# Kernel optimization log

Hardware: AMD Instinct MI355X
Metric: run time of the kernel (lower is better)

Reference implementation:

```python
import jax, jax.numpy as jnp
import numpy as np

B, T = 4, 2048
N_EMBD = 1024
TIME_EMBD = 128
N_HEAD = 16
C_IN = N_EMBD + TIME_EMBD  # 1152


def setup_inputs() -> dict:
    key = jax.random.key(0)
    ks = jax.random.split(key, 7)
    s_in = 1.0 / np.sqrt(C_IN)
    s_e = 1.0 / np.sqrt(N_EMBD)
    return {
        "x": jax.random.normal(ks[0], (B, T, C_IN), jnp.float32),
        "ln_w": jnp.ones((C_IN,), jnp.float32),
        "ln_b": jnp.zeros((C_IN,), jnp.float32),
        "W_attn": jax.random.normal(ks[1], (C_IN, 3 * N_EMBD), jnp.float32) * s_in,
        "b_attn": jax.random.normal(ks[2], (3 * N_EMBD,), jnp.float32) * 0.01,
        "W_proj": jax.random.normal(ks[3], (N_EMBD, N_EMBD), jnp.float32) * s_e,
        "b_proj": jax.random.normal(ks[4], (N_EMBD,), jnp.float32) * 0.01,
    }


def _layernorm(x, w, b, eps=1e-5):
    mu = jnp.mean(x, axis=-1, keepdims=True)
    var = jnp.var(x, axis=-1, keepdims=True)
    return (x - mu) * jax.lax.rsqrt(var + eps) * w + b


def reference(x, ln_w, ln_b, W_attn, b_attn, W_proj, b_proj):
    h = _layernorm(x, ln_w, ln_b)                      # [B,T,C_IN]
    qkv = h @ W_attn + b_attn                          # [B,T,3*N_EMBD]
    q, k, v = jnp.split(qkv, 3, axis=-1)
    hd = N_EMBD // N_HEAD
    q = q.reshape(B, T, N_HEAD, hd).transpose(0, 2, 1, 3)  # [B,H,T,hd]
    k = k.reshape(B, T, N_HEAD, hd).transpose(0, 2, 1, 3)
    v = v.reshape(B, T, N_HEAD, hd).transpose(0, 2, 1, 3)
    att = jnp.einsum("bhqd,bhkd->bhqk", q, k) * (1.0 / np.sqrt(hd))
    mask = jnp.tril(jnp.ones((T, T), bool))
    att = jnp.where(mask, att, -jnp.inf)
    att = jax.nn.softmax(att, axis=-1)                 # dropout p=0 -> identity
    y = jnp.einsum("bhqk,bhkd->bhqd", att, v)          # [B,H,T,hd]
    y = y.transpose(0, 2, 1, 3).reshape(B, T, N_EMBD)
    return y @ W_proj + b_proj
```

## Files before the change

### kernel.cpp

```cpp
#include <hip/hip_runtime.h>
#include <hip/hip_bf16.h>

#define BB 4
#define TT 2048
#define C_IN 1152
#define NE 1024
#define NH 16
#define HD 64
#define MM (BB*TT)
#define N_QKV (3*NE)

typedef __attribute__((ext_vector_type(8))) short s16x8;
typedef __attribute__((ext_vector_type(4))) short s16x4;
typedef __attribute__((ext_vector_type(4))) float f32x4;

static __device__ __forceinline__ unsigned short f2bf(float x) {
    unsigned int u = __float_as_uint(x);
    unsigned int r = (u + 0x7fffu + ((u >> 16) & 1u)) >> 16;
    return (unsigned short)r;
}

static __device__ __forceinline__ void async16(const void* g, void* l) {
    __builtin_amdgcn_global_load_lds((const __attribute__((address_space(1))) void*)g,
                                     (__attribute__((address_space(3))) void*)l, 16, 0, 0);
}

__global__ __launch_bounds__(256) void ln_kernel(const float* __restrict__ x,
                                                 const float* __restrict__ w,
                                                 const float* __restrict__ b,
                                                 unsigned short* __restrict__ h) {
    const int row = blockIdx.x;
    const int tid = threadIdx.x;
    const float4* xr = (const float4*)(x + (size_t)row * C_IN);
    const float4 a0 = xr[tid];
    float4 a1 = make_float4(0.f, 0.f, 0.f, 0.f);
    if (tid < 32) a1 = xr[256 + tid];
    float s  = a0.x + a0.y + a0.z + a0.w + a1.x + a1.y + a1.z + a1.w;
    float sq = a0.x*a0.x + a0.y*a0.y + a0.z*a0.z + a0.w*a0.w
             + a1.x*a1.x + a1.y*a1.y + a1.z*a1.z + a1.w*a1.w;
    for (int off = 1; off < 64; off <<= 1) {
        s  += __shfl_xor(s, off, 64);
        sq += __shfl_xor(sq, off, 64);
    }
    __shared__ float red[2][4];
    const int wid = tid >> 6, lane = tid & 63;
    if (lane == 0) { red[0][wid] = s; red[1][wid] = sq; }
    __syncthreads();
    s  = red[0][0] + red[0][1] + red[0][2] + red[0][3];
    sq = red[1][0] + red[1][1] + red[1][2] + red[1][3];
    const float mu  = s * (1.f / C_IN);
    const float var = sq * (1.f / C_IN) - mu * mu;
    const float rs  = rsqrtf(var + 1e-5f);
    const float4* w4 = (const float4*)w;
    const float4* b4 = (const float4*)b;
    unsigned short* hr = h + (size_t)row * C_IN;
    {
        const float4 wv = w4[tid], bv = b4[tid];
        s16x4 o;
        o[0] = (short)f2bf((a0.x - mu) * rs * wv.x + bv.x);
        o[1] = (short)f2bf((a0.y - mu) * rs * wv.y + bv.y);
        o[2] = (short)f2bf((a0.z - mu) * rs * wv.z + bv.z);
        o[3] = (short)f2bf((a0.w - mu) * rs * wv.w + bv.w);
        *(s16x4*)(hr + tid * 4) = o;
    }
    if (tid < 32) {
        const float4 wv = w4[256 + tid], bv = b4[256 + tid];
        s16x4 o;
        o[0] = (short)f2bf((a1.x - mu) * rs * wv.x + bv.x);
        o[1] = (short)f2bf((a1.y - mu) * rs * wv.y + bv.y);
        o[2] = (short)f2bf((a1.z - mu) * rs * wv.z + bv.z);
        o[3] = (short)f2bf((a1.w - mu) * rs * wv.w + bv.w);
        *(s16x4*)(hr + (256 + tid) * 4) = o;
    }
}

__global__ __launch_bounds__(256) void transpose_cast(const float* __restrict__ in,
                                                      unsigned short* __restrict__ out,
                                                      int K, int N) {
    __shared__ float tile[32][33];
    const int n0 = blockIdx.x * 32, k0 = blockIdx.y * 32;
    const int tx = threadIdx.x & 31, ty = threadIdx.x >> 5;
    for (int i = ty; i < 32; i += 8)
        tile[i][tx] = in[(size_t)(k0 + i) * N + n0 + tx];
    __syncthreads();
    for (int i = ty; i < 32; i += 8)
        out[(size_t)(n0 + i) * K + k0 + tx] = f2bf(tile[tx][i]);
}

#define ATT_SC 0.18033688011112042f

#define EP_STRIDE 136
template <int MODE>
__global__ __launch_bounds__(256) void gemm_bt(const unsigned short* __restrict__ A,
                                               const unsigned short* __restrict__ Bt,
                                               const float* __restrict__ bias,
                                               void* __restrict__ outp,
                                               unsigned short* __restrict__ kb,
                                               unsigned short* __restrict__ vt,
                                               int M, int N, int K) {
    __shared__ unsigned short smem[32768];
    const int tid = threadIdx.x;
    const int wid = tid >> 6, lane = tid & 63;
    const int wm = wid >> 1, wn = wid & 1;
    const int quad = lane >> 4, l16 = lane & 15;

    int m0, n0;
    if (MODE == 0) {
        const int bid = blockIdx.y * gridDim.x + blockIdx.x;
        const int xcd = bid & 7;
        const int k   = bid >> 3;
        const int mg  = k / 96;
        const int r1  = k % 96;
        const int ng  = r1 / 32;
        const int rr  = r1 % 32;
        m0 = (xcd * 8 + mg * 4 + (rr & 3)) * 128;
        n0 = (ng * 8 + (rr >> 2)) * 128;
    } else {
        const int gx  = gridDim.x;
        const int nwg = gx * gridDim.y;
        const int bid = blockIdx.y * gx + blockIdx.x;
        const int wg  = (bid & 7) * (nwg >> 3) + (bid >> 3);
        m0 = (wg / gx) * 128; n0 = (wg % gx) * 128;
    }

    const int rl = lane >> 3;
    const int sc = (lane & 7) ^ rl;
    const unsigned short* gA = A  + (size_t)(m0 + wid * 32 + rl) * K + sc * 8;
    const unsigned short* gB = Bt + (size_t)(n0 + wid * 32 + rl) * K + sc * 8;

    f32x4 acc[4][4] = {};
    const int nk = K >> 6;

    const int sc0 = (quad ^ (l16 & 7)) * 8;
    const int sc1 = ((4 + quad) ^ (l16 & 7)) * 8;

#define STAGE(KT, BUF)                                                          \
    {                                                                           \
        const unsigned short* a_ = gA + (KT) * 64;                              \
        const unsigned short* b_ = gB + (KT) * 64;                              \
        unsigned short* sa_ = &smem[(BUF) * 16384 + wid * 2048];                \
        unsigned short* sb_ = &smem[(BUF) * 16384 + 8192 + wid * 2048];         \
        _Pragma("unroll")                                                       \
        for (int j = 0; j < 4; j++) {                                           \
            async16(a_ + (size_t)(j * 8) * K, sa_ + j * 512);                   \
            async16(b_ + (size_t)(j * 8) * K, sb_ + j * 512);                   \
        }                                                                       \
    }

    STAGE(0, 0);

    for (int kt = 0; kt < nk; kt++) {
        __syncthreads();
        const int cur = kt & 1;
        if (kt + 1 < nk) STAGE(kt + 1, cur ^ 1);

        const unsigned short* As_ = &smem[cur * 16384];
        const unsigned short* Bs_ = &smem[cur * 16384 + 8192];
        #pragma unroll
        for (int h = 0; h < 2; h++) {
            const int sch = h ? sc1 : sc0;
            s16x8 af[4], bfb[4];
            #pragma unroll
            for (int mi = 0; mi < 4; mi++)
                af[mi] = *(const s16x8*)&As_[(wm * 64 + mi * 16 + l16) * 64 + sch];
            #pragma unroll
            for (int ni = 0; ni < 4; ni++)
                bfb[ni] = *(const s16x8*)&Bs_[(wn * 64 + ni * 16 + l16) * 64 + sch];
            #pragma unroll
            for (int mi = 0; mi < 4; mi++)
                #pragma unroll
                for (int ni = 0; ni < 4; ni++)
                    acc[mi][ni] = __builtin_amdgcn_mfma_f32_16x16x32_bf16(af[mi], bfb[ni], acc[mi][ni], 0, 0, 0);
        }
    }
#undef STAGE

    const int which0 = n0 >> 10;
    const float sc_ = (MODE == 0 && which0 == 0) ? ATT_SC : 1.0f;
    for (int ni = 0; ni < 4; ni++) {
        const float bv = bias[n0 + wn * 64 + ni * 16 + l16];
        for (int mi = 0; mi < 4; mi++)
            for (int r = 0; r < 4; r++)
                acc[mi][ni][r] = (acc[mi][ni][r] + bv) * sc_;
    }

    if (MODE == 1) {
        float* Tf = (float*)smem;
        float* out = (float*)outp;
        for (int p = 0; p < 2; p++) {
            __syncthreads();
            if (wm == p) {
                for (int mi = 0; mi < 4; mi++)
                    for (int ni = 0; ni < 4; ni++) {
                        const int col = wn * 64 + ni * 16 + l16;
                        for (int r = 0; r < 4; r++)
                            Tf[(mi * 16 + quad * 4 + r) * 128 + col] = acc[mi][ni][r];
                    }
            }
            __syncthreads();
            const int rlo = tid >> 5;
            const int c4 = (tid & 31) * 4;
            for (int rr2 = rlo; rr2 < 64; rr2 += 8) {
                *(float4*)&out[(size_t)(m0 + p * 64 + rr2) * N + n0 + c4] =
                    *(const float4*)&Tf[rr2 * 128 + c4];
            }
        }
        return;
    }

    const int which = n0 >> 10;
    const int bb = m0 >> 11;
    const int mloc = m0 & 2047;
    unsigned short* T = smem;

    __syncthreads();
    if (which < 2) {
        for (int mi = 0; mi < 4; mi++)
            for (int ni = 0; ni < 4; ni++) {
                const int nl = wn * 64 + ni * 16 + l16;
                for (int r = 0; r < 4; r++)
                    T[(wm * 64 + mi * 16 + quad * 4 + r) * EP_STRIDE + nl] = f2bf(acc[mi][ni][r]);
            }
    } else {
        for (int mi = 0; mi < 4; mi++)
            for (int ni = 0; ni < 4; ni++) {
                const int nlh = wn * 64 + ni * 16 + l16;
                const int mlb = wm * 64 + mi * 16 + quad * 4;
                for (int r = 0; r < 4; r += 2) {
                    const unsigned int pk = (unsigned int)f2bf(acc[mi][ni][r]) |
                                            ((unsigned int)f2bf(acc[mi][ni][r + 1]) << 16);
                    *(unsigned int*)&T[nlh * EP_STRIDE + mlb + r] = pk;
                }
            }
    }
    __syncthreads();

    if (which < 2) {
        unsigned short* qk = (which == 0) ? (unsigned short*)outp : kb;
        const int ml = tid >> 2, c = tid & 3;
        const int nl0 = c * 32;
        const int hh = ((n0 & 1023) >> 6) + (nl0 >> 6);
        const int d0 = nl0 & 63;
        for (int half = 0; half < 2; half++) {
            const int row = half * 64 + ml;
            const int t = mloc + row;
            unsigned short* dst = qk + ((size_t)(bb * 16 + hh) * TT + t) * HD + d0;
            const unsigned short* src = &T[row * EP_STRIDE + nl0];
            for (int u = 0; u < 4; u++)
                *(s16x8*)(dst + u * 8) = *(const s16x8*)(src + u * 8);
        }
    } else {
        const int nlh = tid >> 2, c = tid & 3;
        const int hb = (n0 - 2048) >> 6;
        for (int half = 0; half < 2; half++) {
            const int row = half * 64 + nlh;
            unsigned short* dst = vt + ((size_t)(bb * 16 + hb + half) * HD + nlh) * TT + mloc + c * 32;
            const unsigned short* src = &T[row * EP_STRIDE + c * 32];
            for (int u = 0; u < 4; u++)
                *(s16x8*)(dst + u * 8) = *(const s16x8*)(src + u * 8);
        }
    }
}

#define PST 72

__global__ __launch_bounds__(256) void attn_kernel(const unsigned short* __restrict__ qb,
                                                   const unsigned short* __restrict__ kb,
                                                   const unsigned short* __restrict__ vt,
                                                   unsigned short* __restrict__ yb) {
    __shared__ unsigned short Ks[2][64 * 64];
    __shared__ unsigned short Vs[2][64 * 64];
    __shared__ unsigned short Ps[4][2 * 16 * PST];
    const int tid = threadIdx.x, wid = tid >> 6, lane = tid & 63;
    const int quad = lane >> 4, l16 = lane & 15;
    const int bh = blockIdx.x & 63;
    const int qblk = 15 - (blockIdx.x >> 6);

    const unsigned short* qh = qb + (size_t)bh * TT * HD;
    const unsigned short* kh = kb + (size_t)bh * TT * HD;
    const unsigned short* vh = vt + (size_t)bh * HD * TT;
    unsigned short* ps = Ps[wid];

    const int q0w = qblk * 128 + wid * 32;
    s16x8 aq[2][2];
    #pragma unroll
    for (int mf = 0; mf < 2; mf++) {
        aq[mf][0] = *(const s16x8*)&qh[(size_t)(q0w + mf * 16 + l16) * HD + quad * 8];
        aq[mf][1] = *(const s16x8*)&qh[(size_t)(q0w + mf * 16 + l16) * HD + 32 + quad * 8];
    }
    s16x8 onesf;
    #pragma unroll
    for (int i = 0; i < 8; i++) onesf[i] = (short)0x3F80;

    f32x4 yacc[2][4] = {};
    f32x4 lacc[2] = {};
    const int ntiles = 2 * qblk + 2;

    const int rl = lane >> 3;
    const int cc = (lane & 7) ^ (rl & 7);
    const unsigned short* kp0 = kh + (size_t)(wid * 16 + rl) * HD + cc * 8;
    const unsigned short* kp1 = kh + (size_t)(wid * 16 + 8 + rl) * HD + cc * 8;
    const unsigned short* vp0 = vh + (size_t)(wid * 16 + rl) * TT + cc * 8;
    const unsigned short* vp1 = vh + (size_t)(wid * 16 + 8 + rl) * TT + cc * 8;
    const int ldsK0 = wid * 16 * 64, ldsK1 = (wid * 16 + 8) * 64;

    async16(kp0, &Ks[0][ldsK0]);  async16(kp1, &Ks[0][ldsK1]);
    async16(vp0, &Vs[0][ldsK0]);  async16(vp1, &Vs[0][ldsK1]);
    kp0 += 64 * HD; kp1 += 64 * HD; vp0 += 64; vp1 += 64;

    const int p0s = quad ^ (l16 & 7);
    const int p1s = (4 + quad) ^ (l16 & 7);

#define ATT_STEP(CUR, TT_)                                                              \
    {                                                                                   \
        __syncthreads();                                                                \
        if ((TT_) + 1 < ntiles) {                                                       \
            async16(kp0, &Ks[(CUR) ^ 1][ldsK0]);  async16(kp1, &Ks[(CUR) ^ 1][ldsK1]);  \
            async16(vp0, &Vs[(CUR) ^ 1][ldsK0]);  async16(vp1, &Vs[(CUR) ^ 1][ldsK1]);  \
            kp0 += 64 * HD; kp1 += 64 * HD; vp0 += 64; vp1 += 64;                       \
        }                                                                               \
        const int tk0 = (TT_) * 64;                                                     \
        if (tk0 <= q0w + 31) {                                                          \
            const unsigned short* Kc = Ks[CUR];                                         \
            const unsigned short* Vc = Vs[CUR];                                         \
            s16x8 kf[4][2], vf[4][2];                                                   \
            _Pragma("unroll")                                                           \
            for (int nj = 0; nj < 4; nj++) {                                            \
                kf[nj][0] = *(const s16x8*)&Kc[(nj * 16 + l16) * 64 + p0s * 8];         \
                kf[nj][1] = *(const s16x8*)&Kc[(nj * 16 + l16) * 64 + p1s * 8];         \
            }                                                                           \
            _Pragma("unroll")                                                           \
            for (int ni = 0; ni < 4; ni++) {                                            \
                vf[ni][0] = *(const s16x8*)&Vc[(ni * 16 + l16) * 64 + p0s * 8];         \
                vf[ni][1] = *(const s16x8*)&Vc[(ni * 16 + l16) * 64 + p1s * 8];         \
            }                                                                           \
            _Pragma("unroll")                                                           \
            for (int mf = 0; mf < 2; mf++) {                                            \
                const int f0 = q0w + mf * 16;                                           \
                if (tk0 > f0 + 15) continue;                                            \
                unsigned short* pm = ps + mf * (16 * PST);                              \
                const int qg = f0 + l16;                                                \
                f32x4 st[4];                                                            \
                _Pragma("unroll")                                                       \
                for (int nj = 0; nj < 4; nj++) {                                        \
                    f32x4 z = {};                                                       \
                    z = __builtin_amdgcn_mfma_f32_16x16x32_bf16(kf[nj][0], aq[mf][0], z, 0, 0, 0); \
                    z = __builtin_amdgcn_mfma_f32_16x16x32_bf16(kf[nj][1], aq[mf][1], z, 0, 0, 0); \
                    st[nj] = z;                                                         \
                }                                                                       \
                const bool diag = (tk0 + 64 > f0);                                      \
                float pv[4][4];                                                         \
                _Pragma("unroll")                                                       \
                for (int nj = 0; nj < 4; nj++)                                          \
                    _Pragma("unroll")                                                   \
                    for (int r = 0; r < 4; r++)                                         \
                        pv[nj][r] = exp2f(st[nj][r]);                                   \
                if (diag) {                                                             \
                    _Pragma("unroll")                                                   \
                    for (int nj = 0; nj < 4; nj++) {                                    \
                        const int keyb = tk0 + nj * 16 + quad * 4;                      \
                        _Pragma("unroll")                                               \
                        for (int r = 0; r < 4; r++)                                     \
                            if (keyb + r > qg) pv[nj][r] = 0.f;                         \
                    }                                                                   \
                }                                                                       \
                _Pragma("unroll")                                                       \
                for (int nj = 0; nj < 4; nj++) {                                        \
                    const unsigned int pk0 = __builtin_amdgcn_perm(                     \
                        __float_as_uint(pv[nj][1]), __float_as_uint(pv[nj][0]), 0x07060302u); \
                    const unsigned int pk1 = __builtin_amdgcn_perm(                     \
                        __float_as_uint(pv[nj][3]), __float_as_uint(pv[nj][2]), 0x07060302u); \
                    *(uint2*)&pm[l16 * PST + nj * 16 + quad * 4] = make_uint2(pk0, pk1);\
                }                                                                       \
                __asm volatile("s_waitcnt lgkmcnt(0)" ::: "memory");                    \
                __builtin_amdgcn_s_setprio(1);                                          \
                const s16x8 ap0 = *(const s16x8*)&pm[l16 * PST + quad * 8];             \
                const s16x8 ap1 = *(const s16x8*)&pm[l16 * PST + 32 + quad * 8];        \
                lacc[mf] = __builtin_amdgcn_mfma_f32_16x16x32_bf16(ap0, onesf, lacc[mf], 0, 0, 0); \
                lacc[mf] = __builtin_amdgcn_mfma_f32_16x16x32_bf16(ap1, onesf, lacc[mf], 0, 0, 0); \
                _Pragma("unroll")                                                       \
                for (int ni = 0; ni < 4; ni++) {                                        \
                    yacc[mf][ni] = __builtin_amdgcn_mfma_f32_16x16x32_bf16(ap0, vf[ni][0], yacc[mf][ni], 0, 0, 0); \
                    yacc[mf][ni] = __builtin_amdgcn_mfma_f32_16x16x32_bf16(ap1, vf[ni][1], yacc[mf][ni], 0, 0, 0); \
                }                                                                       \
                __builtin_amdgcn_s_setprio(0);                                          \
            }                                                                           \
        }                                                                               \
    }

    for (int t = 0; t < ntiles; t += 2) {
        ATT_STEP(0, t);
        ATT_STEP(1, t + 1);
    }
#undef ATT_STEP

    const int bbi = bh >> 4, hh = bh & 15;
    #pragma unroll
    for (int mf = 0; mf < 2; mf++) {
        float linv[4];
        #pragma unroll
        for (int r = 0; r < 4; r++)
            linv[r] = 1.0f / lacc[mf][r];
        #pragma unroll
        for (int ni = 0; ni < 4; ni++)
            #pragma unroll
            for (int r = 0; r < 4; r++) {
                const int trow = q0w + mf * 16 + quad * 4 + r;
                yb[((size_t)bbi * TT + trow) * NE + hh * HD + ni * 16 + l16] =
                    f2bf(yacc[mf][ni][r] * linv[r]);
            }
    }
}

extern "C" void kernel_launch(void* const* d_in, const int* in_sizes, int n_in,
                              void* d_out, int out_size, void* d_ws, size_t ws_size,
                              hipStream_t stream) {
    const float* x      = (const float*)d_in[0];
    const float* ln_w   = (const float*)d_in[1];
    const float* ln_b   = (const float*)d_in[2];
    const float* W_attn = (const float*)d_in[3];
    const float* b_attn = (const float*)d_in[4];
    const float* W_proj = (const float*)d_in[5];
    const float* b_proj = (const float*)d_in[6];
    float* out = (float*)d_out;

    char* ws = (char*)d_ws;
    unsigned short* h    = (unsigned short*)ws;  ws += (size_t)MM * C_IN * 2;
    unsigned short* Wat  = (unsigned short*)ws;  ws += (size_t)N_QKV * C_IN * 2;
    unsigned short* Wpt  = (unsigned short*)ws;  ws += (size_t)NE * NE * 2;
    unsigned short* qbuf = (unsigned short*)ws;  ws += (size_t)MM * NE * 2;
    unsigned short* kbuf = (unsigned short*)ws;  ws += (size_t)MM * NE * 2;
    unsigned short* vtbf = (unsigned short*)ws;  ws += (size_t)MM * NE * 2;
    unsigned short* ybuf = (unsigned short*)ws;  ws += (size_t)MM * NE * 2;

    ln_kernel<<<MM, 256, 0, stream>>>(x, ln_w, ln_b, h);
    transpose_cast<<<dim3(N_QKV / 32, C_IN / 32), 256, 0, stream>>>(W_attn, Wat, C_IN, N_QKV);
    transpose_cast<<<dim3(NE / 32, NE / 32), 256, 0, stream>>>(W_proj, Wpt, NE, NE);
    gemm_bt<0><<<dim3(N_QKV / 128, MM / 128), 256, 0, stream>>>(h, Wat, b_attn, qbuf, kbuf, vtbf,
                                                                MM, N_QKV, C_IN);
    attn_kernel<<<64 * 16, 256, 0, stream>>>(qbuf, kbuf, vtbf, ybuf);
    gemm_bt<1><<<dim3(NE / 128, MM / 128), 256, 0, stream>>>(ybuf, Wpt, b_proj, out, nullptr, nullptr,
                                                             MM, NE, NE);
}
```

Before: 288.6 us.

## Merge prep kernels and enlarge attention blocks to 256 queries with 8 waves

LayerNorm and both weight transpose-casts now run in a single launch that dispatches on block index. The attention kernel moves from 256 to 512 threads (8 waves), so each block covers 256 query rows and shares each K/V tile across twice as many waves. The grid shrinks to 512 blocks with a reordered q-block schedule, and each thread issues one async K and one async V load per tile. This halves K/V global traffic per query and removes two launches, at the cost of coarser load balancing across the causal triangle and fewer resident blocks.

```diff
diff --git a/kernel.cpp b/kernel.cpp
--- a/kernel.cpp
+++ b/kernel.cpp
@@ -25,61 +25,76 @@
                                      (__attribute__((address_space(3))) void*)l, 16, 0, 0);
 }
 
-__global__ __launch_bounds__(256) void ln_kernel(const float* __restrict__ x,
-                                                 const float* __restrict__ w,
-                                                 const float* __restrict__ b,
-                                                 unsigned short* __restrict__ h) {
-    const int row = blockIdx.x;
+#define TCA_BLOCKS ((N_QKV / 32) * (C_IN / 32))
+#define TCP_BLOCKS ((NE / 32) * (NE / 32))
+__global__ __launch_bounds__(256) void prep_kernel(const float* __restrict__ x,
+                                                   const float* __restrict__ lw,
+                                                   const float* __restrict__ lb,
+                                                   unsigned short* __restrict__ h,
+                                                   const float* __restrict__ Wa,
+                                                   unsigned short* __restrict__ Wat,
+                                                   const float* __restrict__ Wp,
+                                                   unsigned short* __restrict__ Wpt) {
+    __shared__ float tile[32][33];
+    __shared__ float red[2][4];
+    const int bid = blockIdx.x;
     const int tid = threadIdx.x;
-    const float4* xr = (const float4*)(x + (size_t)row * C_IN);
-    const float4 a0 = xr[tid];
-    float4 a1 = make_float4(0.f, 0.f, 0.f, 0.f);
-    if (tid < 32) a1 = xr[256 + tid];
-    float s  = a0.x + a0.y + a0.z + a0.w + a1.x + a1.y + a1.z + a1.w;
-    float sq = a0.x*a0.x + a0.y*a0.y + a0.z*a0.z + a0.w*a0.w
-             + a1.x*a1.x + a1.y*a1.y + a1.z*a1.z + a1.w*a1.w;
-    for (int off = 1; off < 64; off <<= 1) {
-        s  += __shfl_xor(s, off, 64);
-        sq += __shfl_xor(sq, off, 64);
-    }
-    __shared__ float red[2][4];
-    const int wid = tid >> 6, lane = tid & 63;
-    if (lane == 0) { red[0][wid] = s; red[1][wid] = sq; }
-    __syncthreads();
-    s  = red[0][0] + red[0][1] + red[0][2] + red[0][3];
-    sq = red[1][0] + red[1][1] + red[1][2] + red[1][3];
-    const float mu  = s * (1.f / C_IN);
-    const float var = sq * (1.f / C_IN) - mu * mu;
-    const float rs  = rsqrtf(var + 1e-5f);
-    const float4* w4 = (const float4*)w;
-    const float4* b4 = (const float4*)b;
-    unsigned short* hr = h + (size_t)row * C_IN;
-    {
-        const float4 wv = w4[tid], bv = b4[tid];
-        s16x4 o;
-        o[0] = (short)f2bf((a0.x - mu) * rs * wv.x + bv.x);
-        o[1] = (short)f2bf((a0.y - mu) * rs * wv.y + bv.y);
-        o[2] = (short)f2bf((a0.z - mu) * rs * wv.z + bv.z);
-        o[3] = (short)f2bf((a0.w - mu) * rs * wv.w + bv.w);
-        *(s16x4*)(hr + tid * 4) = o;
-    }
-    if (tid < 32) {
-        const float4 wv = w4[256 + tid], bv = b4[256 + tid];
-        s16x4 o;
-        o[0] = (short)f2bf((a1.x - mu) * rs * wv.x + bv.x);
-        o[1] = (short)f2bf((a1.y - mu) * rs * wv.y + bv.y);
-        o[2] = (short)f2bf((a1.z - mu) * rs * wv.z + bv.z);
-        o[3] = (short)f2bf((a1.w - mu) * rs * wv.w + bv.w);
-        *(s16x4*)(hr + (256 + tid) * 4) = o;
-    }
-}
-
-__global__ __launch_bounds__(256) void transpose_cast(const float* __restrict__ in,
-                                                      unsigned short* __restrict__ out,
-                                                      int K, int N) {
-    __shared__ float tile[32][33];
-    const int n0 = blockIdx.x * 32, k0 = blockIdx.y * 32;
-    const int tx = threadIdx.x & 31, ty = threadIdx.x >> 5;
+
+    if (bid < MM) {
+        const float4* xr = (const float4*)(x + (size_t)bid * C_IN);
+        const float4 a0 = xr[tid];
+        float4 a1 = make_float4(0.f, 0.f, 0.f, 0.f);
+        if (tid < 32) a1 = xr[256 + tid];
+        float s  = a0.x + a0.y + a0.z + a0.w + a1.x + a1.y + a1.z + a1.w;
+        float sq = a0.x*a0.x + a0.y*a0.y + a0.z*a0.z + a0.w*a0.w
+                 + a1.x*a1.x + a1.y*a1.y + a1.z*a1.z + a1.w*a1.w;
+        for (int off = 1; off < 64; off <<= 1) {
+            s  += __shfl_xor(s, off, 64);
+            sq += __shfl_xor(sq, off, 64);
+        }
+        const int wid = tid >> 6, lane = tid & 63;
+        if (lane == 0) { red[0][wid] = s; red[1][wid] = sq; }
+        __syncthreads();
+        s  = red[0][0] + red[0][1] + red[0][2] + red[0][3];
+        sq = red[1][0] + red[1][1] + red[1][2] + red[1][3];
+        const float mu  = s * (1.f / C_IN);
+        const float var = sq * (1.f / C_IN) - mu * mu;
+        const float rs  = rsqrtf(var + 1e-5f);
+        const float4* w4 = (const float4*)lw;
+        const float4* b4 = (const float4*)lb;
+        unsigned short* hr = h + (size_t)bid * C_IN;
+        {
+            const float4 wv = w4[tid], bv = b4[tid];
+            s16x4 o;
+            o[0] = (short)f2bf((a0.x - mu) * rs * wv.x + bv.x);
+            o[1] = (short)f2bf((a0.y - mu) * rs * wv.y + bv.y);
+            o[2] = (short)f2bf((a0.z - mu) * rs * wv.z + bv.z);
+            o[3] = (short)f2bf((a0.w - mu) * rs * wv.w + bv.w);
+            *(s16x4*)(hr + tid * 4) = o;
+        }
+        if (tid < 32) {
+            const float4 wv = w4[256 + tid], bv = b4[256 + tid];
+            s16x4 o;
+            o[0] = (short)f2bf((a1.x - mu) * rs * wv.x + bv.x);
+            o[1] = (short)f2bf((a1.y - mu) * rs * wv.y + bv.y);
+            o[2] = (short)f2bf((a1.z - mu) * rs * wv.z + bv.z);
+            o[3] = (short)f2bf((a1.w - mu) * rs * wv.w + bv.w);
+            *(s16x4*)(hr + (256 + tid) * 4) = o;
+        }
+        return;
+    }
+
+    const float* in; unsigned short* out; int K, N, n0, k0;
+    if (bid < MM + TCA_BLOCKS) {
+        const int idx = bid - MM;
+        in = Wa; out = Wat; K = C_IN; N = N_QKV;
+        n0 = (idx % (N_QKV / 32)) * 32; k0 = (idx / (N_QKV / 32)) * 32;
+    } else {
+        const int idx = bid - MM - TCA_BLOCKS;
+        in = Wp; out = Wpt; K = NE; N = NE;
+        n0 = (idx % (NE / 32)) * 32; k0 = (idx / (NE / 32)) * 32;
+    }
+    const int tx = tid & 31, ty = tid >> 5;
     for (int i = ty; i < 32; i += 8)
         tile[i][tx] = in[(size_t)(k0 + i) * N + n0 + tx];
     __syncthreads();
@@ -264,24 +279,25 @@
 
 #define PST 72
 
-__global__ __launch_bounds__(256) void attn_kernel(const unsigned short* __restrict__ qb,
+__global__ __launch_bounds__(512) void attn_kernel(const unsigned short* __restrict__ qb,
                                                    const unsigned short* __restrict__ kb,
                                                    const unsigned short* __restrict__ vt,
                                                    unsigned short* __restrict__ yb) {
     __shared__ unsigned short Ks[2][64 * 64];
     __shared__ unsigned short Vs[2][64 * 64];
-    __shared__ unsigned short Ps[4][2 * 16 * PST];
+    __shared__ unsigned short Ps[8][2 * 16 * PST];
     const int tid = threadIdx.x, wid = tid >> 6, lane = tid & 63;
     const int quad = lane >> 4, l16 = lane & 15;
     const int bh = blockIdx.x & 63;
-    const int qblk = 15 - (blockIdx.x >> 6);
+    const int qidx = blockIdx.x >> 6;
+    const int qblk = (qidx < 4) ? (7 - qidx) : (qidx - 4);
 
     const unsigned short* qh = qb + (size_t)bh * TT * HD;
     const unsigned short* kh = kb + (size_t)bh * TT * HD;
     const unsigned short* vh = vt + (size_t)bh * HD * TT;
     unsigned short* ps = Ps[wid];
 
-    const int q0w = qblk * 128 + wid * 32;
+    const int q0w = qblk * 256 + wid * 32;
     s16x8 aq[2][2];
     #pragma unroll
     for (int mf = 0; mf < 2; mf++) {
@@ -294,19 +310,17 @@
 
     f32x4 yacc[2][4] = {};
     f32x4 lacc[2] = {};
-    const int ntiles = 2 * qblk + 2;
+    const int ntiles = 4 * qblk + 4;
 
     const int rl = lane >> 3;
-    const int cc = (lane & 7) ^ (rl & 7);
-    const unsigned short* kp0 = kh + (size_t)(wid * 16 + rl) * HD + cc * 8;
-    const unsigned short* kp1 = kh + (size_t)(wid * 16 + 8 + rl) * HD + cc * 8;
-    const unsigned short* vp0 = vh + (size_t)(wid * 16 + rl) * TT + cc * 8;
-    const unsigned short* vp1 = vh + (size_t)(wid * 16 + 8 + rl) * TT + cc * 8;
-    const int ldsK0 = wid * 16 * 64, ldsK1 = (wid * 16 + 8) * 64;
-
-    async16(kp0, &Ks[0][ldsK0]);  async16(kp1, &Ks[0][ldsK1]);
-    async16(vp0, &Vs[0][ldsK0]);  async16(vp1, &Vs[0][ldsK1]);
-    kp0 += 64 * HD; kp1 += 64 * HD; vp0 += 64; vp1 += 64;
+    const int cc = (lane & 7) ^ rl;
+    const unsigned short* kp0 = kh + (size_t)(wid * 8 + rl) * HD + cc * 8;
+    const unsigned short* vp0 = vh + (size_t)(wid * 8 + rl) * TT + cc * 8;
+    const int ldsF = wid * 512;
+
+    async16(kp0, &Ks[0][ldsF]);
+    async16(vp0, &Vs[0][ldsF]);
+    kp0 += 64 * HD; vp0 += 64;
 
     const int p0s = quad ^ (l16 & 7);
     const int p1s = (4 + quad) ^ (l16 & 7);
@@ -315,9 +329,9 @@
     {                                                                                   \
         __syncthreads();                                                                \
         if ((TT_) + 1 < ntiles) {                                                       \
-            async16(kp0, &Ks[(CUR) ^ 1][ldsK0]);  async16(kp1, &Ks[(CUR) ^ 1][ldsK1]);  \
-            async16(vp0, &Vs[(CUR) ^ 1][ldsK0]);  async16(vp1, &Vs[(CUR) ^ 1][ldsK1]);  \
-            kp0 += 64 * HD; kp1 += 64 * HD; vp0 += 64; vp1 += 64;                       \
+            async16(kp0, &Ks[(CUR) ^ 1][ldsF]);                                         \
+            async16(vp0, &Vs[(CUR) ^ 1][ldsF]);                                         \
+            kp0 += 64 * HD; vp0 += 64;                                                  \
         }                                                                               \
         const int tk0 = (TT_) * 64;                                                     \
         if (tk0 <= q0w + 31) {                                                          \
@@ -433,12 +447,11 @@
     unsigned short* vtbf = (unsigned short*)ws;  ws += (size_t)MM * NE * 2;
     unsigned short* ybuf = (unsigned short*)ws;  ws += (size_t)MM * NE * 2;
 
-    ln_kernel<<<MM, 256, 0, stream>>>(x, ln_w, ln_b, h);
-    transpose_cast<<<dim3(N_QKV / 32, C_IN / 32), 256, 0, stream>>>(W_attn, Wat, C_IN, N_QKV);
-    transpose_cast<<<dim3(NE / 32, NE / 32), 256, 0, stream>>>(W_proj, Wpt, NE, NE);
+    prep_kernel<<<MM + TCA_BLOCKS + TCP_BLOCKS, 256, 0, stream>>>(x, ln_w, ln_b, h,
+                                                                  W_attn, Wat, W_proj, Wpt);
     gemm_bt<0><<<dim3(N_QKV / 128, MM / 128), 256, 0, stream>>>(h, Wat, b_attn, qbuf, kbuf, vtbf,
                                                                 MM, N_QKV, C_IN);
-    attn_kernel<<<64 * 16, 256, 0, stream>>>(qbuf, kbuf, vtbf, ybuf);
+    attn_kernel<<<64 * 8, 512, 0, stream>>>(qbuf, kbuf, vtbf, ybuf);
     gemm_bt<1><<<dim3(NE / 128, MM / 128), 256, 0, stream>>>(ybuf, Wpt, b_proj, out, nullptr, nullptr,
                                                              MM, NE, NE);
 }
```

Result: no change. 287.6 us (-0.3%).
